# Kernel optimization log

Measured on AMD Instinct MI355X. Metric: run time of the kernel, lower is better.

The kernel has to match this reference:

```python
import jax, jax.numpy as jnp
import numpy as np

GAMMA = 0.5
POLY_COEF = 0.1
POLY_DEGREE = 3


def setup_inputs() -> dict:
    key = jax.random.key(0)
    kx, ky = jax.random.split(key)
    x = jax.random.normal(kx, (8192, 256), dtype=jnp.float32)
    y = jax.random.normal(ky, (8192, 256), dtype=jnp.float32)
    return {"x": x, "y": y}


def reference(x, y):
    # K(x, y) = exp(-gamma * ||x - y||^2) + poly_coef * (x.y^T + 1)^degree
    xy = x @ y.T                                   # (N, M) GEMM
    x2 = jnp.sum(x * x, axis=-1, keepdims=True)    # (N, 1)
    y2 = jnp.sum(y * y, axis=-1)[None, :]          # (1, M)
    sqdist = jnp.maximum(x2 + y2 - 2.0 * xy, 0.0)
    rbf = jnp.exp(-GAMMA * sqdist)
    poly = POLY_COEF * (xy + 1.0) ** POLY_DEGREE
    return rbf + poly
```

## Files before the change

kernel.cpp:

```cpp
#include <hip/hip_runtime.h>
#include <hip/hip_bf16.h>
#include <cstdint>
#include <cstddef>


#define NROWS 8192
#define DK    256
#define BM    128
#define BN    128
#define BK    32

typedef __bf16 bf16_8 __attribute__((ext_vector_type(8)));
typedef float  f32x4  __attribute__((ext_vector_type(4)));

__device__ __forceinline__ unsigned short f2bf(float f) {
    unsigned int u = __builtin_bit_cast(unsigned int, f);
    u = (u + 0x7FFFu + ((u >> 16) & 1u)) >> 16;
    return (unsigned short)u;
}

__global__ __launch_bounds__(64) void prep_kernel(
    const float* __restrict__ x, const float* __restrict__ y,
    unsigned short* __restrict__ xb, unsigned short* __restrict__ yb,
    float* __restrict__ x2, float* __restrict__ y2)
{
    const int row  = blockIdx.x;
    const int lane = threadIdx.x;
    const size_t base = (size_t)row * DK + lane * 4;

    const float4 vx = *(const float4*)(x + base);
    const float4 vy = *(const float4*)(y + base);

    ushort4 hx = make_ushort4(f2bf(vx.x), f2bf(vx.y), f2bf(vx.z), f2bf(vx.w));
    ushort4 hy = make_ushort4(f2bf(vy.x), f2bf(vy.y), f2bf(vy.z), f2bf(vy.w));
    *(ushort4*)(xb + base) = hx;
    *(ushort4*)(yb + base) = hy;

    float sx = vx.x * vx.x + vx.y * vx.y + vx.z * vx.z + vx.w * vx.w;
    float sy = vy.x * vy.x + vy.y * vy.y + vy.z * vy.z + vy.w * vy.w;
    #pragma unroll
    for (int off = 32; off > 0; off >>= 1) {
        sx += __shfl_down(sx, off);
        sy += __shfl_down(sy, off);
    }
    if (lane == 0) {
        x2[row] = sx;
        y2[row] = sy;
    }
}

__global__ __launch_bounds__(256) void gemm_ep_kernel(
    const unsigned short* __restrict__ xb, const unsigned short* __restrict__ yb,
    const float* __restrict__ x2, const float* __restrict__ y2,
    float* __restrict__ out)
{
    __shared__ __align__(16) unsigned short As[BM * BK];
    __shared__ __align__(16) unsigned short Bs[BN * BK];

    const int tid  = threadIdx.x;
    const int wave = tid >> 6;
    const int lane = tid & 63;
    const int bm   = blockIdx.x;
    const int bn   = blockIdx.y;

    const int wm = (wave & 1) * 64;
    const int wn = (wave >> 1) * 64;

    const int c0   = wave * 2;
    const int c1   = c0 + 1;
    const int lrow = lane >> 2;
    const int lcol = (lane & 3) * 8;

    const unsigned short* gA0 = xb + (size_t)(bm * BM + c0 * 16 + lrow) * DK + lcol;
    const unsigned short* gA1 = xb + (size_t)(bm * BM + c1 * 16 + lrow) * DK + lcol;
    const unsigned short* gB0 = yb + (size_t)(bn * BN + c0 * 16 + lrow) * DK + lcol;
    const unsigned short* gB1 = yb + (size_t)(bn * BN + c1 * 16 + lrow) * DK + lcol;
    unsigned short* lA0 = &As[c0 * 512];
    unsigned short* lA1 = &As[c1 * 512];
    unsigned short* lB0 = &Bs[c0 * 512];
    unsigned short* lB1 = &Bs[c1 * 512];

    f32x4 acc[4][4];
    #pragma unroll
    for (int i = 0; i < 4; ++i)
        #pragma unroll
        for (int j = 0; j < 4; ++j)
            acc[i][j] = (f32x4){0.f, 0.f, 0.f, 0.f};

    const int quad = lane >> 4;
    const int l15  = lane & 15;

    for (int kt = 0; kt < DK; kt += BK) {
        __builtin_amdgcn_global_load_lds(
            (const __attribute__((address_space(1))) void*)(gA0 + kt),
            (__attribute__((address_space(3))) void*)lA0, 16, 0, 0);
        __builtin_amdgcn_global_load_lds(
            (const __attribute__((address_space(1))) void*)(gA1 + kt),
            (__attribute__((address_space(3))) void*)lA1, 16, 0, 0);
        __builtin_amdgcn_global_load_lds(
            (const __attribute__((address_space(1))) void*)(gB0 + kt),
            (__attribute__((address_space(3))) void*)lB0, 16, 0, 0);
        __builtin_amdgcn_global_load_lds(
            (const __attribute__((address_space(1))) void*)(gB1 + kt),
            (__attribute__((address_space(3))) void*)lB1, 16, 0, 0);
        __syncthreads();

        bf16_8 afr[4], bfr[4];
        #pragma unroll
        for (int i = 0; i < 4; ++i)
            afr[i] = *(const bf16_8*)&As[(wm + i * 16 + l15) * BK + quad * 8];
        #pragma unroll
        for (int j = 0; j < 4; ++j)
            bfr[j] = *(const bf16_8*)&Bs[(wn + j * 16 + l15) * BK + quad * 8];

        #pragma unroll
        for (int i = 0; i < 4; ++i)
            #pragma unroll
            for (int j = 0; j < 4; ++j)
                acc[i][j] = __builtin_amdgcn_mfma_f32_16x16x32_bf16(
                    afr[i], bfr[j], acc[i][j], 0, 0, 0);
        __syncthreads();
    }

    const int mBase = bm * BM + wm + quad * 4;
    const int nBase = bn * BN + wn + l15;

    float y2v[4];
    #pragma unroll
    for (int j = 0; j < 4; ++j) y2v[j] = y2[nBase + j * 16];

    #pragma unroll
    for (int i = 0; i < 4; ++i) {
        #pragma unroll
        for (int r = 0; r < 4; ++r) {
            const int m = mBase + i * 16 + r;
            const float xv = x2[m];
            float* orow = out + (size_t)m * NROWS + nBase;
            #pragma unroll
            for (int j = 0; j < 4; ++j) {
                const float xy = acc[i][j][r];
                float s = xv + y2v[j] - 2.0f * xy;
                s = fmaxf(s, 0.0f);
                const float e = __expf(-0.5f * s);
                const float p = xy + 1.0f;
                orow[j * 16] = fmaf(0.1f, p * p * p, e);
            }
        }
    }
}

extern "C" void kernel_launch(void* const* d_in, const int* in_sizes, int n_in,
                              void* d_out, int out_size, void* d_ws, size_t ws_size,
                              hipStream_t stream) {
    const float* x = (const float*)d_in[0];
    const float* y = (const float*)d_in[1];
    float* out = (float*)d_out;

    char* ws = (char*)d_ws;
    unsigned short* xb = (unsigned short*)ws;
    unsigned short* yb = (unsigned short*)(ws + (size_t)NROWS * DK * 2);
    float* x2 = (float*)(ws + (size_t)2 * NROWS * DK * 2);
    float* y2 = x2 + NROWS;

    prep_kernel<<<NROWS, 64, 0, stream>>>(x, y, xb, yb, x2, y2);

    dim3 grid(NROWS / BM, NROWS / BN);
    gemm_ep_kernel<<<grid, 256, 0, stream>>>(xb, yb, x2, y2, out);
}
```

Before: 296.6 us.

## Pre-swizzle bf16 operands into MFMA fragment layout and load fragments directly from global

The prep kernel now writes the bf16 copies of x and y in a tiled layout that matches the MFMA 16x16x32 fragment order, 16 rows per block, and reduces the row norms across waves through LDS. The GEMM kernel drops LDS staging and its barriers and has each wave read its fragments straight from global memory with contiguous 16-byte loads. This removes LDS traffic and __syncthreads. In exchange, operand reuse between waves now depends on L1/L2 caching instead of shared memory.

```diff
diff --git a/kernel.cpp b/kernel.cpp
--- a/kernel.cpp
+++ b/kernel.cpp
@@ -8,10 +8,10 @@
 #define DK    256
 #define BM    128
 #define BN    128
-#define BK    32
 
 typedef __bf16 bf16_8 __attribute__((ext_vector_type(8)));
 typedef float  f32x4  __attribute__((ext_vector_type(4)));
+typedef unsigned short us8 __attribute__((ext_vector_type(8)));
 
 __device__ __forceinline__ unsigned short f2bf(float f) {
     unsigned int u = __builtin_bit_cast(unsigned int, f);
@@ -19,33 +19,73 @@
     return (unsigned short)u;
 }
 
-__global__ __launch_bounds__(64) void prep_kernel(
+__global__ __launch_bounds__(256) void prep_kernel(
     const float* __restrict__ x, const float* __restrict__ y,
     unsigned short* __restrict__ xb, unsigned short* __restrict__ yb,
     float* __restrict__ x2, float* __restrict__ y2)
 {
-    const int row  = blockIdx.x;
-    const int lane = threadIdx.x;
-    const size_t base = (size_t)row * DK + lane * 4;
+    const int p    = blockIdx.x;
+    const int t    = threadIdx.x;
+    const int r    = t & 15;
+    const int g    = t >> 4;
+    const int c0   = g >> 2;
+    const int quad = g & 3;
+    const int wave = t >> 6;
+    const int lane = t & 63;
 
-    const float4 vx = *(const float4*)(x + base);
-    const float4 vy = *(const float4*)(y + base);
+    __shared__ float redx[4][16];
+    __shared__ float redy[4][16];
 
-    ushort4 hx = make_ushort4(f2bf(vx.x), f2bf(vx.y), f2bf(vx.z), f2bf(vx.w));
-    ushort4 hy = make_ushort4(f2bf(vy.x), f2bf(vy.y), f2bf(vy.z), f2bf(vy.w));
-    *(ushort4*)(xb + base) = hx;
-    *(ushort4*)(yb + base) = hy;
+    const size_t row = (size_t)p * 16 + r;
+    const size_t rb0 = row * DK + c0 * 32 + quad * 8;
+    const size_t rb1 = rb0 + 128;
 
-    float sx = vx.x * vx.x + vx.y * vx.y + vx.z * vx.z + vx.w * vx.w;
-    float sy = vy.x * vy.x + vy.y * vy.y + vy.z * vy.z + vy.w * vy.w;
-    #pragma unroll
-    for (int off = 32; off > 0; off >>= 1) {
-        sx += __shfl_down(sx, off);
-        sy += __shfl_down(sy, off);
+    const size_t d0 = ((size_t)(p * 8 + c0) * 512) + (size_t)(quad * 16 + r) * 8;
+    const size_t d1 = d0 + 4 * 512;
+
+    float sx, sy;
+    {
+        float4 v0 = *(const float4*)(x + rb0);
+        float4 v1 = *(const float4*)(x + rb0 + 4);
+        float4 v2 = *(const float4*)(x + rb1);
+        float4 v3 = *(const float4*)(x + rb1 + 4);
+        us8 h0 = {f2bf(v0.x), f2bf(v0.y), f2bf(v0.z), f2bf(v0.w),
+                  f2bf(v1.x), f2bf(v1.y), f2bf(v1.z), f2bf(v1.w)};
+        us8 h1 = {f2bf(v2.x), f2bf(v2.y), f2bf(v2.z), f2bf(v2.w),
+                  f2bf(v3.x), f2bf(v3.y), f2bf(v3.z), f2bf(v3.w)};
+        *(us8*)(xb + d0) = h0;
+        *(us8*)(xb + d1) = h1;
+        sx = v0.x*v0.x + v0.y*v0.y + v0.z*v0.z + v0.w*v0.w
+           + v1.x*v1.x + v1.y*v1.y + v1.z*v1.z + v1.w*v1.w
+           + v2.x*v2.x + v2.y*v2.y + v2.z*v2.z + v2.w*v2.w
+           + v3.x*v3.x + v3.y*v3.y + v3.z*v3.z + v3.w*v3.w;
     }
-    if (lane == 0) {
-        x2[row] = sx;
-        y2[row] = sy;
+    {
+        float4 v0 = *(const float4*)(y + rb0);
+        float4 v1 = *(const float4*)(y + rb0 + 4);
+        float4 v2 = *(const float4*)(y + rb1);
+        float4 v3 = *(const float4*)(y + rb1 + 4);
+        us8 h0 = {f2bf(v0.x), f2bf(v0.y), f2bf(v0.z), f2bf(v0.w),
+                  f2bf(v1.x), f2bf(v1.y), f2bf(v1.z), f2bf(v1.w)};
+        us8 h1 = {f2bf(v2.x), f2bf(v2.y), f2bf(v2.z), f2bf(v2.w),
+                  f2bf(v3.x), f2bf(v3.y), f2bf(v3.z), f2bf(v3.w)};
+        *(us8*)(yb + d0) = h0;
+        *(us8*)(yb + d1) = h1;
+        sy = v0.x*v0.x + v0.y*v0.y + v0.z*v0.z + v0.w*v0.w
+           + v1.x*v1.x + v1.y*v1.y + v1.z*v1.z + v1.w*v1.w
+           + v2.x*v2.x + v2.y*v2.y + v2.z*v2.z + v2.w*v2.w
+           + v3.x*v3.x + v3.y*v3.y + v3.z*v3.z + v3.w*v3.w;
+    }
+
+    sx += __shfl_xor(sx, 16); sx += __shfl_xor(sx, 32);
+    sy += __shfl_xor(sy, 16); sy += __shfl_xor(sy, 32);
+    if (lane < 16) { redx[wave][lane] = sx; redy[wave][lane] = sy; }
+    __syncthreads();
+    if (t < 16) {
+        x2[(size_t)p * 16 + t] = redx[0][t] + redx[1][t] + redx[2][t] + redx[3][t];
+    } else if (t < 32) {
+        const int rr = t - 16;
+        y2[(size_t)p * 16 + rr] = redy[0][rr] + redy[1][rr] + redy[2][rr] + redy[3][rr];
     }
 }
 
@@ -54,31 +94,16 @@
     const float* __restrict__ x2, const float* __restrict__ y2,
     float* __restrict__ out)
 {
-    __shared__ __align__(16) unsigned short As[BM * BK];
-    __shared__ __align__(16) unsigned short Bs[BN * BK];
-
     const int tid  = threadIdx.x;
     const int wave = tid >> 6;
     const int lane = tid & 63;
     const int bm   = blockIdx.x;
     const int bn   = blockIdx.y;
+    const int wm   = (wave & 1) * 64;
+    const int wn   = (wave >> 1) * 64;
 
-    const int wm = (wave & 1) * 64;
-    const int wn = (wave >> 1) * 64;
-
-    const int c0   = wave * 2;
-    const int c1   = c0 + 1;
-    const int lrow = lane >> 2;
-    const int lcol = (lane & 3) * 8;
-
-    const unsigned short* gA0 = xb + (size_t)(bm * BM + c0 * 16 + lrow) * DK + lcol;
-    const unsigned short* gA1 = xb + (size_t)(bm * BM + c1 * 16 + lrow) * DK + lcol;
-    const unsigned short* gB0 = yb + (size_t)(bn * BN + c0 * 16 + lrow) * DK + lcol;
-    const unsigned short* gB1 = yb + (size_t)(bn * BN + c1 * 16 + lrow) * DK + lcol;
-    unsigned short* lA0 = &As[c0 * 512];
-    unsigned short* lA1 = &As[c1 * 512];
-    unsigned short* lB0 = &Bs[c0 * 512];
-    unsigned short* lB1 = &Bs[c1 * 512];
+    const unsigned short* aB = xb + ((size_t)(bm * 8 + (wm >> 4)) * 8) * 512 + (size_t)lane * 8;
+    const unsigned short* bB = yb + ((size_t)(bn * 8 + (wn >> 4)) * 8) * 512 + (size_t)lane * 8;
 
     f32x4 acc[4][4];
     #pragma unroll
@@ -87,41 +112,25 @@
         for (int j = 0; j < 4; ++j)
             acc[i][j] = (f32x4){0.f, 0.f, 0.f, 0.f};
 
-    const int quad = lane >> 4;
-    const int l15  = lane & 15;
-
-    for (int kt = 0; kt < DK; kt += BK) {
-        __builtin_amdgcn_global_load_lds(
-            (const __attribute__((address_space(1))) void*)(gA0 + kt),
-            (__attribute__((address_space(3))) void*)lA0, 16, 0, 0);
-        __builtin_amdgcn_global_load_lds(
-            (const __attribute__((address_space(1))) void*)(gA1 + kt),
-            (__attribute__((address_space(3))) void*)lA1, 16, 0, 0);
-        __builtin_amdgcn_global_load_lds(
-            (const __attribute__((address_space(1))) void*)(gB0 + kt),
-            (__attribute__((address_space(3))) void*)lB0, 16, 0, 0);
-        __builtin_amdgcn_global_load_lds(
-            (const __attribute__((address_space(1))) void*)(gB1 + kt),
-            (__attribute__((address_space(3))) void*)lB1, 16, 0, 0);
-        __syncthreads();
-
+    #pragma unroll
+    for (int c = 0; c < 8; ++c) {
         bf16_8 afr[4], bfr[4];
         #pragma unroll
         for (int i = 0; i < 4; ++i)
-            afr[i] = *(const bf16_8*)&As[(wm + i * 16 + l15) * BK + quad * 8];
+            afr[i] = *(const bf16_8*)(aB + i * 4096 + c * 512);
         #pragma unroll
         for (int j = 0; j < 4; ++j)
-            bfr[j] = *(const bf16_8*)&Bs[(wn + j * 16 + l15) * BK + quad * 8];
-
+            bfr[j] = *(const bf16_8*)(bB + j * 4096 + c * 512);
         #pragma unroll
         for (int i = 0; i < 4; ++i)
             #pragma unroll
             for (int j = 0; j < 4; ++j)
                 acc[i][j] = __builtin_amdgcn_mfma_f32_16x16x32_bf16(
                     afr[i], bfr[j], acc[i][j], 0, 0, 0);
-        __syncthreads();
     }
 
+    const int quad  = lane >> 4;
+    const int l15   = lane & 15;
     const int mBase = bm * BM + wm + quad * 4;
     const int nBase = bn * BN + wn + l15;
 
@@ -162,7 +171,7 @@
     float* x2 = (float*)(ws + (size_t)2 * NROWS * DK * 2);
     float* y2 = x2 + NROWS;
 
-    prep_kernel<<<NROWS, 64, 0, stream>>>(x, y, xb, yb, x2, y2);
+    prep_kernel<<<NROWS / 16, 256, 0, stream>>>(x, y, xb, yb, x2, y2);
 
     dim3 grid(NROWS / BM, NROWS / BN);
     gemm_ep_kernel<<<grid, 256, 0, stream>>>(xb, yb, x2, y2, out);
```

Measured after the change: 310.6 us. 1.05x slower.

## Double K-tile depth, XOR-swizzle LDS layout, and group blocks into supertiles

Applied to the files above, without the earlier changes.

Raises the K tile from 32 to 64, which halves the number of barrier-separated iterations. It stores A/B tiles in LDS with an XOR swizzle on the 16-byte column blocks so fragment reads avoid bank conflicts. It also replaces the 2D grid with a 1D grid mapped into 16x16 supertiles to improve L2 reuse of the bf16 inputs. The cost is twice the LDS per block, which may reduce occupancy, and more address arithmetic.

```diff
diff --git a/kernel.cpp b/kernel.cpp
--- a/kernel.cpp
+++ b/kernel.cpp
@@ -8,7 +8,7 @@
 #define DK    256
 #define BM    128
 #define BN    128
-#define BK    32
+#define BKK   64
 
 typedef __bf16 bf16_8 __attribute__((ext_vector_type(8)));
 typedef float  f32x4  __attribute__((ext_vector_type(4)));
@@ -54,31 +54,30 @@
     const float* __restrict__ x2, const float* __restrict__ y2,
     float* __restrict__ out)
 {
-    __shared__ __align__(16) unsigned short As[BM * BK];
-    __shared__ __align__(16) unsigned short Bs[BN * BK];
+    __shared__ __align__(16) unsigned short As[BM * BKK];
+    __shared__ __align__(16) unsigned short Bs[BN * BKK];
 
     const int tid  = threadIdx.x;
     const int wave = tid >> 6;
     const int lane = tid & 63;
-    const int bm   = blockIdx.x;
-    const int bn   = blockIdx.y;
+
+    const int id  = blockIdx.x;
+    const int sup = id >> 8;
+    const int loc = id & 255;
+    const int bm  = (sup & 3) * 16 + (loc >> 4);
+    const int bn  = (sup >> 2) * 16 + (loc & 15);
 
     const int wm = (wave & 1) * 64;
     const int wn = (wave >> 1) * 64;
 
-    const int c0   = wave * 2;
-    const int c1   = c0 + 1;
-    const int lrow = lane >> 2;
-    const int lcol = (lane & 3) * 8;
+    const int r8 = lane >> 3;
+    const int cb = lane & 7;
+    const int scol = (cb ^ r8) * 8;
 
-    const unsigned short* gA0 = xb + (size_t)(bm * BM + c0 * 16 + lrow) * DK + lcol;
-    const unsigned short* gA1 = xb + (size_t)(bm * BM + c1 * 16 + lrow) * DK + lcol;
-    const unsigned short* gB0 = yb + (size_t)(bn * BN + c0 * 16 + lrow) * DK + lcol;
-    const unsigned short* gB1 = yb + (size_t)(bn * BN + c1 * 16 + lrow) * DK + lcol;
-    unsigned short* lA0 = &As[c0 * 512];
-    unsigned short* lA1 = &As[c1 * 512];
-    unsigned short* lB0 = &Bs[c0 * 512];
-    unsigned short* lB1 = &Bs[c1 * 512];
+    const unsigned short* gA = xb + (size_t)(bm * BM + wave * 32 + r8) * DK + scol;
+    const unsigned short* gB = yb + (size_t)(bn * BN + wave * 32 + r8) * DK + scol;
+    unsigned short* lA = &As[wave * 4 * 512 + lane * 8];
+    unsigned short* lB = &Bs[wave * 4 * 512 + lane * 8];
 
     f32x4 acc[4][4];
     #pragma unroll
@@ -89,36 +88,37 @@
 
     const int quad = lane >> 4;
     const int l15  = lane & 15;
+    const int sw   = l15 & 7;
 
-    for (int kt = 0; kt < DK; kt += BK) {
-        __builtin_amdgcn_global_load_lds(
-            (const __attribute__((address_space(1))) void*)(gA0 + kt),
-            (__attribute__((address_space(3))) void*)lA0, 16, 0, 0);
-        __builtin_amdgcn_global_load_lds(
-            (const __attribute__((address_space(1))) void*)(gA1 + kt),
-            (__attribute__((address_space(3))) void*)lA1, 16, 0, 0);
-        __builtin_amdgcn_global_load_lds(
-            (const __attribute__((address_space(1))) void*)(gB0 + kt),
-            (__attribute__((address_space(3))) void*)lB0, 16, 0, 0);
-        __builtin_amdgcn_global_load_lds(
-            (const __attribute__((address_space(1))) void*)(gB1 + kt),
-            (__attribute__((address_space(3))) void*)lB1, 16, 0, 0);
+    for (int kt = 0; kt < 4; ++kt) {
+        #pragma unroll
+        for (int c = 0; c < 4; ++c) {
+            __builtin_amdgcn_global_load_lds(
+                (const __attribute__((address_space(1))) void*)(gA + kt * 64 + c * 8 * DK),
+                (__attribute__((address_space(3))) void*)(lA + c * 512), 16, 0, 0);
+            __builtin_amdgcn_global_load_lds(
+                (const __attribute__((address_space(1))) void*)(gB + kt * 64 + c * 8 * DK),
+                (__attribute__((address_space(3))) void*)(lB + c * 512), 16, 0, 0);
+        }
         __syncthreads();
 
-        bf16_8 afr[4], bfr[4];
         #pragma unroll
-        for (int i = 0; i < 4; ++i)
-            afr[i] = *(const bf16_8*)&As[(wm + i * 16 + l15) * BK + quad * 8];
-        #pragma unroll
-        for (int j = 0; j < 4; ++j)
-            bfr[j] = *(const bf16_8*)&Bs[(wn + j * 16 + l15) * BK + quad * 8];
-
-        #pragma unroll
-        for (int i = 0; i < 4; ++i)
+        for (int s = 0; s < 2; ++s) {
+            bf16_8 afr[4], bfr[4];
+            const int blk = ((s * 4 + quad) ^ sw) * 8;
+            #pragma unroll
+            for (int i = 0; i < 4; ++i)
+                afr[i] = *(const bf16_8*)&As[(wm + i * 16 + l15) * BKK + blk];
             #pragma unroll
             for (int j = 0; j < 4; ++j)
-                acc[i][j] = __builtin_amdgcn_mfma_f32_16x16x32_bf16(
-                    afr[i], bfr[j], acc[i][j], 0, 0, 0);
+                bfr[j] = *(const bf16_8*)&Bs[(wn + j * 16 + l15) * BKK + blk];
+            #pragma unroll
+            for (int i = 0; i < 4; ++i)
+                #pragma unroll
+                for (int j = 0; j < 4; ++j)
+                    acc[i][j] = __builtin_amdgcn_mfma_f32_16x16x32_bf16(
+                        afr[i], bfr[j], acc[i][j], 0, 0, 0);
+        }
         __syncthreads();
     }
 
@@ -164,6 +164,5 @@
 
     prep_kernel<<<NROWS, 64, 0, stream>>>(x, y, xb, yb, x2, y2);
 
-    dim3 grid(NROWS / BM, NROWS / BN);
-    gemm_ep_kernel<<<grid, 256, 0, stream>>>(xb, yb, x2, y2, out);
+    gemm_ep_kernel<<<4096, 256, 0, stream>>>(xb, yb, x2, y2, out);
 }
```

Result: no change. 296.8 us (+0.1%).
